# Kernel optimization log

Hardware: AMD Instinct MI355X
Metric: run time of the kernel (lower is better)

Reference implementation:

```python
import jax, jax.numpy as jnp
import numpy as np

M, K, N = 4096, 4096, 11008  # tokens, in_features, out_features
PACK = 8  # int4 nibbles per int32


def setup_inputs() -> dict:
    key = jax.random.key(0)
    k1, k2, k3, k4, k5 = jax.random.split(key, 5)
    x = jax.random.normal(k1, (M, K), dtype=jnp.float32)
    weights = jax.random.randint(k2, (N, K // PACK), 0, 2147483647, dtype=jnp.int32)
    # positive per-channel scales, small float zero offsets (GPTQ-style affine)
    scales = jax.random.uniform(k3, (N,), dtype=jnp.float32, minval=0.005, maxval=0.02)
    zeros = jax.random.normal(k4, (N,), dtype=jnp.float32) * 0.05
    bias = jax.random.normal(k5, (N,), dtype=jnp.float32) * 0.02
    return {"x": x, "weights": weights, "scales": scales, "zeros": zeros, "bias": bias}


def _unpack_int4(weights):
    # weights: [N, K//8] int32 -> nibbles [N, K] in [0, 15]
    shifts = jnp.arange(PACK, dtype=jnp.int32) * 4  # [8]
    nib = (weights[:, :, None] >> shifts[None, None, :]) & 0xF  # [N, K//8, 8]
    return nib.reshape(weights.shape[0], -1)  # [N, K]


def reference(x, weights, scales, zeros, bias):
    x_dtype = x.dtype
    xb = x.astype(jnp.bfloat16)
    q = _unpack_int4(weights).astype(jnp.bfloat16)  # [N, K]
    # dequant: w = q * scale + zero  (per output channel)
    w = q * scales.astype(jnp.bfloat16)[:, None] + zeros.astype(jnp.bfloat16)[:, None]
    out = jnp.einsum('mk,nk->mn', xb, w, preferred_element_type=jnp.float32)
    out = out + bias[None, :]
    return out.astype(x_dtype)
```

## Files before the change

### kernel.cpp

```cpp
#include <hip/hip_runtime.h>
#include <stdint.h>

#define MDIM 4096
#define KDIM 4096
#define NDIM 11008
#define KP   (KDIM/8)
#define NKT2 (KDIM/128)

typedef float  f32x4   __attribute__((ext_vector_type(4)));
typedef __bf16 bf16x8  __attribute__((ext_vector_type(8)));
typedef unsigned short u16x8 __attribute__((ext_vector_type(8)));
typedef int    i32x4   __attribute__((ext_vector_type(4)));
typedef int    i32x16  __attribute__((ext_vector_type(16)));
typedef char   c8x8    __attribute__((ext_vector_type(8)));
typedef char   c8x16   __attribute__((ext_vector_type(16)));

__device__ __forceinline__ unsigned short f2bf(float f) {
  uint32_t u = __builtin_bit_cast(uint32_t, f);
  u += 0x7FFFu + ((u >> 16) & 1u);
  return (unsigned short)(u >> 16);
}
__device__ __forceinline__ float bf2f(unsigned short h) {
  return __builtin_bit_cast(float, (uint32_t)h << 16);
}
__device__ __forceinline__ float bf16r(float f) { return bf2f(f2bf(f)); }

__device__ __forceinline__ void lds16(const void* g, void* l) {
  __builtin_amdgcn_global_load_lds(
      (const __attribute__((address_space(1))) unsigned int*)g,
      (__attribute__((address_space(3))) unsigned int*)l, 16, 0, 0);
}

__global__ __launch_bounds__(256) void repack_q_kernel(
    const uint32_t* __restrict__ wq, c8x8* __restrict__ Q8) {
  int idx = blockIdx.x * 256 + threadIdx.x;
  uint32_t w = wq[idx];
  c8x8 v;
#pragma unroll
  for (int j = 0; j < 8; ++j) v[j] = (char)((w >> (4 * j)) & 0xF);
  Q8[idx] = v;
}

__global__ __launch_bounds__(256) void quant_x_kernel(
    const float* __restrict__ x, c8x16* __restrict__ X8,
    float* __restrict__ delta, float* __restrict__ xsum) {
  __shared__ float red[256];
  const int row = blockIdx.x, t = threadIdx.x;
  const float4* xr = (const float4*)(x + (size_t)row * KDIM);
  float xb[16];
#pragma unroll
  for (int i = 0; i < 4; ++i) {
    float4 f = xr[t * 4 + i];
    xb[i * 4 + 0] = bf16r(f.x); xb[i * 4 + 1] = bf16r(f.y);
    xb[i * 4 + 2] = bf16r(f.z); xb[i * 4 + 3] = bf16r(f.w);
  }
  float mx = 0.f, sm = 0.f;
#pragma unroll
  for (int j = 0; j < 16; ++j) { mx = fmaxf(mx, fabsf(xb[j])); sm += xb[j]; }
  red[t] = mx; __syncthreads();
  for (int o = 128; o > 0; o >>= 1) {
    if (t < o) red[t] = fmaxf(red[t], red[t + o]);
    __syncthreads();
  }
  const float rmx = red[0];
  __syncthreads();
  red[t] = sm; __syncthreads();
  for (int o = 128; o > 0; o >>= 1) {
    if (t < o) red[t] += red[t + o];
    __syncthreads();
  }
  const float rsm = red[0];
  const float inv = (rmx > 0.f) ? 127.0f / rmx : 0.f;
  if (t == 0) {
    delta[row] = (rmx > 0.f) ? rmx / 127.0f : 0.f;
    xsum[row]  = rsm;
  }
  c8x16 q;
#pragma unroll
  for (int j = 0; j < 16; ++j) q[j] = (char)__float2int_rn(xb[j] * inv);
  X8[(size_t)row * 256 + t] = q;
}

__global__ __launch_bounds__(512, 2) void gemm256_i8_kernel(
    const char* __restrict__ A8, const char* __restrict__ Q8,
    const float* __restrict__ delta, const float* __restrict__ xsum,
    const float* __restrict__ scales, const float* __restrict__ zeros,
    const float* __restrict__ bias, float* __restrict__ out) {
  __shared__ __align__(16) char smem[131072];

  const int tid  = threadIdx.x;
  const int lane = tid & 63;
  const int wave = tid >> 6;
  const int wm   = wave >> 2;
  const int wn   = wave & 3;

  const int b   = blockIdx.x;
  const int swz = (b & 7) * 86 + (b >> 3);
  const int mt  = swz / 43;
  const int nt  = swz - mt * 43;
  const int bm0 = mt * 256, bn0 = nt * 256;

  const int srow   = lane >> 2;
  const int schunk = lane & 3;
  const int perm0  = schunk ^ (((srow >> 3) & 1) << 1);
  const int perm1  = perm0 ^ 1;
  const char* aR  = A8 + (size_t)(bm0 + wave * 32 + srow) * KDIM + perm0 * 16;
  const char* aR2 = A8 + (size_t)(bm0 + wave * 32 + 16 + srow) * KDIM + perm1 * 16;
  const char* bR  = Q8 + (size_t)(bn0 + wave * 32 + srow) * KDIM + perm0 * 16;
  const char* bR2 = Q8 + (size_t)(bn0 + wave * 32 + 16 + srow) * KDIM + perm1 * 16;

  const int r31 = lane & 31;
  const int sub = r31 >> 4;
  const int r15 = r31 & 15;
  const int hk  = lane >> 5;
  const int rd0 = sub * 1024 + r15 * 64 + ((hk ^ sub) << 4) + ((r15 & 8) << 2);
  const int rd1 = rd0 ^ 32;

  const int aoffc = wm * 8192;
  const int boffc = 65536 + wn * 4096;

  i32x16 acc[4][2];
#pragma unroll
  for (int i = 0; i < 4; ++i)
#pragma unroll
    for (int j = 0; j < 2; ++j)
#pragma unroll
      for (int r = 0; r < 16; ++r) acc[i][j][r] = 0;

  i32x4 Af[4], Bf[2];

#define STAGE_A(tile, h, slot)                                              \
  do {                                                                      \
    const size_t ko_ = (size_t)((tile) * 128 + (h) * 64);                   \
    char* d_ = smem + ((slot) << 14) + wave * 2048;                         \
    lds16(aR + ko_, d_);                                                    \
    lds16(aR2 + ko_, d_ + 1024);                                            \
  } while (0)

#define STAGE_B(tile, h, slot)                                              \
  do {                                                                      \
    const size_t ko_ = (size_t)((tile) * 128 + (h) * 64);                   \
    char* d_ = smem + 65536 + ((slot) << 14) + wave * 2048;                 \
    lds16(bR + ko_, d_);                                                    \
    lds16(bR2 + ko_, d_ + 1024);                                            \
  } while (0)

#define READ6(slotbase, S)                                                  \
  do {                                                                      \
    const int ro_ = (S) ? rd1 : rd0;                                        \
    _Pragma("unroll") for (int mf = 0; mf < 4; ++mf)                        \
        Af[mf] = *(const i32x4*)(smem + aoffc + (slotbase) +                \
                                 mf * 2048 + ro_);                          \
    _Pragma("unroll") for (int nf = 0; nf < 2; ++nf)                        \
        Bf[nf] = *(const i32x4*)(smem + boffc + (slotbase) +                \
                                 nf * 2048 + ro_);                          \
  } while (0)

#define MFMA8()                                                             \
  __builtin_amdgcn_s_setprio(1);                                            \
  _Pragma("unroll") for (int mf = 0; mf < 4; ++mf)                          \
      _Pragma("unroll") for (int nf = 0; nf < 2; ++nf)                      \
          acc[mf][nf] = __builtin_amdgcn_mfma_i32_32x32x32_i8(              \
              Af[mf], Bf[nf], acc[mf][nf], 0, 0, 0);                        \
  __builtin_amdgcn_s_setprio(0);

#define BAR                                                                 \
  __builtin_amdgcn_s_barrier();                                             \
  __builtin_amdgcn_sched_barrier(0);

#define VMWAIT(N) asm volatile("s_waitcnt vmcnt(" #N ")" ::: "memory")

#define TILE(T, S0s, S1s, SN1s, NSTG, VM1STMT, VM3STMT)                     \
  do {                                                                      \
    READ6((S0s) << 14, 0);                                                  \
    if ((NSTG) >= 1) STAGE_A((T) + 1, 1, SN1s);                             \
    BAR; MFMA8(); BAR;                                                      \
    READ6((S0s) << 14, 1);                                                  \
    if ((NSTG) >= 2) STAGE_B((T) + 1, 1, SN1s);                             \
    VM1STMT;                                                                \
    BAR; MFMA8(); BAR;                                                      \
    READ6((S1s) << 14, 0);                                                  \
    if ((NSTG) >= 3) STAGE_A((T) + 2, 0, S0s);                              \
    BAR; MFMA8(); BAR;                                                      \
    READ6((S1s) << 14, 1);                                                  \
    if ((NSTG) >= 4) STAGE_B((T) + 2, 0, S0s);                              \
    VM3STMT;                                                                \
    BAR; MFMA8(); BAR;                                                      \
  } while (0)

  STAGE_A(0, 0, 0);
  STAGE_B(0, 0, 0);
  STAGE_A(0, 1, 1);
  STAGE_B(0, 1, 1);
  STAGE_A(1, 0, 2);
  STAGE_B(1, 0, 2);
  VMWAIT(8);
  BAR;

  for (int tt = 0; tt < 30; tt += 2) {
    TILE(tt,     0, 1, 3, 4, VMWAIT(8), VMWAIT(8));
    TILE(tt + 1, 2, 3, 1, 4, VMWAIT(8), VMWAIT(8));
  }
  TILE(30, 0, 1, 3, 2, VMWAIT(8), VMWAIT(4));
  TILE(31, 2, 3, 1, 0, VMWAIT(0), (void)0);

#undef TILE
#undef VMWAIT
#undef BAR
#undef MFMA8
#undef READ6
#undef STAGE_B
#undef STAGE_A

  const int colv = bn0 + wn * 64 + (lane & 31);
  const int rowb = bm0 + wm * 128 + ((lane >> 5) << 2);
  float sb[2], zb[2], bv[2];
#pragma unroll
  for (int nf = 0; nf < 2; ++nf) {
    sb[nf] = bf16r(scales[colv + nf * 32]);
    zb[nf] = bf16r(zeros[colv + nf * 32]);
    bv[nf] = bias[colv + nf * 32];
  }
#pragma unroll
  for (int mf = 0; mf < 4; ++mf)
#pragma unroll
    for (int reg = 0; reg < 16; ++reg) {
      const int row = rowb + mf * 32 + (reg & 3) + ((reg >> 2) << 3);
      const float dm = delta[row];
      const float xm = xsum[row];
#pragma unroll
      for (int nf = 0; nf < 2; ++nf)
        out[(size_t)row * NDIM + colv + nf * 32] =
            (float)acc[mf][nf][reg] * (dm * sb[nf]) + (zb[nf] * xm + bv[nf]);
    }
}

__global__ __launch_bounds__(256, 3) void gemm_fused_kernel(
    const float* __restrict__ x, const uint32_t* __restrict__ wq,
    const float* __restrict__ scales, const float* __restrict__ zeros,
    const float* __restrict__ bias, float* __restrict__ out) {
  __shared__ __align__(16) char smem[2 * 128 * 64 * 2];
  char* As = smem;
  char* Bs = smem + 16384;

  const int tid  = threadIdx.x;
  const int lane = tid & 63;
  const int wave = tid >> 6;
  const int wm = wave >> 1, wn = wave & 1;

  const int b   = blockIdx.x;
  const int swz = (b & 7) * 344 + (b >> 3);
  const int mt  = swz / 86;
  const int nt  = swz - mt * 86;
  const int bm0 = mt * 128, bn0 = nt * 128;

  f32x4 acc[4][4];
#pragma unroll
  for (int i = 0; i < 4; ++i)
#pragma unroll
    for (int j = 0; j < 4; ++j) acc[i][j] = (f32x4){0.f, 0.f, 0.f, 0.f};

  const int base_a = ((wm * 64 + (lane & 15)) << 7) + ((lane >> 4) << 4);
  const int base_b = ((wn * 64 + (lane & 15)) << 7) + ((lane >> 4) << 4);

  float sv[4], zv[4];
#pragma unroll
  for (int it = 0; it < 4; ++it) {
    int r = bn0 + it * 32 + (tid >> 3);
    sv[it] = bf16r(scales[r]);
    zv[it] = bf16r(zeros[r]);
  }

  for (int kt = 0; kt < KDIM / 64; ++kt) {
    const int k0 = kt * 64;
    __syncthreads();
#pragma unroll
    for (int it = 0; it < 4; ++it) {
      int ch = it * 256 + tid;
      int row = ch >> 3, c8 = ch & 7;
      const float* src = x + (size_t)(bm0 + row) * KDIM + k0 + c8 * 8;
      float4 f0 = *(const float4*)src;
      float4 f1 = *(const float4*)(src + 4);
      u16x8 v;
      v[0] = f2bf(f0.x); v[1] = f2bf(f0.y); v[2] = f2bf(f0.z); v[3] = f2bf(f0.w);
      v[4] = f2bf(f1.x); v[5] = f2bf(f1.y); v[6] = f2bf(f1.z); v[7] = f2bf(f1.w);
      *(u16x8*)(As + row * 128 + c8 * 16) = v;
    }
#pragma unroll
    for (int it = 0; it < 4; ++it) {
      int ch = it * 256 + tid;
      int row = ch >> 3, kp = ch & 7;
      uint32_t w = wq[(size_t)(bn0 + row) * KP + kt * 8 + kp];
      float s = sv[it], z = zv[it];
      u16x8 v;
#pragma unroll
      for (int j = 0; j < 8; ++j) {
        float qf = (float)((w >> (4 * j)) & 0xF);
        float t  = bf16r(qf * s);
        v[j] = f2bf(t + z);
      }
      *(u16x8*)(Bs + row * 128 + kp * 16) = v;
    }
    __syncthreads();
#pragma unroll
    for (int ks = 0; ks < 2; ++ks) {
      bf16x8 af[4], bf[4];
#pragma unroll
      for (int i = 0; i < 4; ++i)
        af[i] = *(const bf16x8*)(As + base_a + i * 2048 + ks * 64);
#pragma unroll
      for (int j = 0; j < 4; ++j)
        bf[j] = *(const bf16x8*)(Bs + base_b + j * 2048 + ks * 64);
#pragma unroll
      for (int i = 0; i < 4; ++i)
#pragma unroll
        for (int j = 0; j < 4; ++j)
          acc[i][j] = __builtin_amdgcn_mfma_f32_16x16x32_bf16(af[i], bf[j],
                                                              acc[i][j], 0, 0, 0);
    }
  }

  const int colbase = bn0 + wn * 64 + (lane & 15);
  const int rowbase = bm0 + wm * 64 + ((lane >> 4) << 2);
  float bv[4];
#pragma unroll
  for (int j = 0; j < 4; ++j) bv[j] = bias[colbase + j * 16];
#pragma unroll
  for (int i = 0; i < 4; ++i) {
#pragma unroll
    for (int j = 0; j < 4; ++j) {
      size_t base = (size_t)(rowbase + i * 16) * NDIM + colbase + j * 16;
#pragma unroll
      for (int r = 0; r < 4; ++r)
        out[base + (size_t)r * NDIM] = acc[i][j][r] + bv[j];
    }
  }
}

extern "C" void kernel_launch(void* const* d_in, const int* in_sizes, int n_in,
                              void* d_out, int out_size, void* d_ws, size_t ws_size,
                              hipStream_t stream) {
  const float*    x      = (const float*)d_in[0];
  const uint32_t* wq     = (const uint32_t*)d_in[1];
  const float*    scales = (const float*)d_in[2];
  const float*    zeros  = (const float*)d_in[3];
  const float*    bias   = (const float*)d_in[4];
  float*          out    = (float*)d_out;

  const size_t offQ = 0;
  const size_t szQ  = (size_t)NDIM * KDIM;
  const size_t offX = szQ;
  const size_t szX  = (size_t)MDIM * KDIM;
  const size_t offD = offX + szX;
  const size_t offS = offD + MDIM * sizeof(float);
  const size_t need = offS + MDIM * sizeof(float);

  if (ws_size >= need) {
    char*  Q8    = (char*)d_ws + offQ;
    char*  X8    = (char*)d_ws + offX;
    float* dlt   = (float*)((char*)d_ws + offD);
    float* xsm   = (float*)((char*)d_ws + offS);
    repack_q_kernel<<<(NDIM * KP) / 256, 256, 0, stream>>>(wq, (c8x8*)Q8);
    quant_x_kernel<<<MDIM, 256, 0, stream>>>(x, (c8x16*)X8, dlt, xsm);
    gemm256_i8_kernel<<<688, 512, 0, stream>>>(X8, Q8, dlt, xsm, scales, zeros,
                                               bias, out);
  } else {
    gemm_fused_kernel<<<2752, 256, 0, stream>>>(x, wq, scales, zeros, bias, out);
  }
}
```

Before: 232.4 us.

## Shrink int8 GEMM block tile to 128x256 with triple-buffered LDS pipeline

Changes the int8 MFMA GEMM block tile from 256x256 to 128x256. Each wave now holds a 2x2 set of 32x32 accumulators instead of 4x2, and LDS use drops from 128KB to 72KB. The pipeline becomes a 3-slot rotation that prefetches one full K-tile ahead, and launch bounds ask for more resident blocks with twice as many blocks launched. The aim is higher occupancy and better wave balance across CUs, at the cost of more global traffic for B per output and a lower MFMA-to-load ratio per block.

```diff
diff --git a/kernel.cpp b/kernel.cpp
--- a/kernel.cpp
+++ b/kernel.cpp
@@ -5,7 +5,6 @@
 #define KDIM 4096
 #define NDIM 11008
 #define KP   (KDIM/8)
-#define NKT2 (KDIM/128)
 
 typedef float  f32x4   __attribute__((ext_vector_type(4)));
 typedef __bf16 bf16x8  __attribute__((ext_vector_type(8)));
@@ -81,12 +80,12 @@
   X8[(size_t)row * 256 + t] = q;
 }
 
-__global__ __launch_bounds__(512, 2) void gemm256_i8_kernel(
+__global__ __launch_bounds__(512, 4) void gemm_i8_kernel(
     const char* __restrict__ A8, const char* __restrict__ Q8,
     const float* __restrict__ delta, const float* __restrict__ xsum,
     const float* __restrict__ scales, const float* __restrict__ zeros,
     const float* __restrict__ bias, float* __restrict__ out) {
-  __shared__ __align__(16) char smem[131072];
+  __shared__ __align__(16) char smem[73728];
 
   const int tid  = threadIdx.x;
   const int lane = tid & 63;
@@ -95,19 +94,20 @@
   const int wn   = wave & 3;
 
   const int b   = blockIdx.x;
-  const int swz = (b & 7) * 86 + (b >> 3);
+  const int swz = (b & 7) * 172 + (b >> 3);
   const int mt  = swz / 43;
   const int nt  = swz - mt * 43;
-  const int bm0 = mt * 256, bn0 = nt * 256;
+  const int bm0 = mt * 128, bn0 = nt * 256;
 
   const int srow   = lane >> 2;
   const int schunk = lane & 3;
-  const int perm0  = schunk ^ (((srow >> 3) & 1) << 1);
-  const int perm1  = perm0 ^ 1;
-  const char* aR  = A8 + (size_t)(bm0 + wave * 32 + srow) * KDIM + perm0 * 16;
-  const char* aR2 = A8 + (size_t)(bm0 + wave * 32 + 16 + srow) * KDIM + perm1 * 16;
-  const char* bR  = Q8 + (size_t)(bn0 + wave * 32 + srow) * KDIM + perm0 * 16;
-  const char* bR2 = Q8 + (size_t)(bn0 + wave * 32 + 16 + srow) * KDIM + perm1 * 16;
+  const int p0c    = schunk ^ (((srow >> 3) & 1) << 1);
+  const char* aRw = A8 + (size_t)(bm0 + wave * 16 + srow) * KDIM
+                       + (size_t)((p0c ^ (wave & 1)) * 16);
+  const char* bR  = Q8 + (size_t)(bn0 + wave * 32 + srow) * KDIM
+                       + (size_t)(p0c * 16);
+  const char* bR2 = Q8 + (size_t)(bn0 + wave * 32 + 16 + srow) * KDIM
+                       + (size_t)((p0c ^ 1) * 16);
 
   const int r31 = lane & 31;
   const int sub = r31 >> 4;
@@ -116,49 +116,48 @@
   const int rd0 = sub * 1024 + r15 * 64 + ((hk ^ sub) << 4) + ((r15 & 8) << 2);
   const int rd1 = rd0 ^ 32;
 
-  const int aoffc = wm * 8192;
-  const int boffc = 65536 + wn * 4096;
-
-  i32x16 acc[4][2];
-#pragma unroll
-  for (int i = 0; i < 4; ++i)
+  const int apair = (wm << 1);
+  const int bpair = (wn << 1);
+
+  i32x16 acc[2][2];
+#pragma unroll
+  for (int i = 0; i < 2; ++i)
 #pragma unroll
     for (int j = 0; j < 2; ++j)
 #pragma unroll
       for (int r = 0; r < 16; ++r) acc[i][j][r] = 0;
 
-  i32x4 Af[4], Bf[2];
+  i32x4 Af[2], Bf[2];
+
+#define ABASE(S) ((S) * 8192)
+#define BBASE(S) (24576 + (S) * 16384)
 
 #define STAGE_A(tile, h, slot)                                              \
-  do {                                                                      \
-    const size_t ko_ = (size_t)((tile) * 128 + (h) * 64);                   \
-    char* d_ = smem + ((slot) << 14) + wave * 2048;                         \
-    lds16(aR + ko_, d_);                                                    \
-    lds16(aR2 + ko_, d_ + 1024);                                            \
-  } while (0)
+  lds16(aRw + (size_t)((tile) * 128 + (h) * 64),                            \
+        smem + ABASE(slot) + wave * 1024)
 
 #define STAGE_B(tile, h, slot)                                              \
   do {                                                                      \
     const size_t ko_ = (size_t)((tile) * 128 + (h) * 64);                   \
-    char* d_ = smem + 65536 + ((slot) << 14) + wave * 2048;                 \
+    char* d_ = smem + BBASE(slot) + wave * 2048;                            \
     lds16(bR + ko_, d_);                                                    \
     lds16(bR2 + ko_, d_ + 1024);                                            \
   } while (0)
 
-#define READ6(slotbase, S)                                                  \
+#define READ4(S, KS)                                                        \
   do {                                                                      \
-    const int ro_ = (S) ? rd1 : rd0;                                        \
-    _Pragma("unroll") for (int mf = 0; mf < 4; ++mf)                        \
-        Af[mf] = *(const i32x4*)(smem + aoffc + (slotbase) +                \
-                                 mf * 2048 + ro_);                          \
+    const int ro_ = (KS) ? rd1 : rd0;                                       \
+    _Pragma("unroll") for (int mf = 0; mf < 2; ++mf)                        \
+        Af[mf] = *(const i32x4*)(smem + ABASE(S) +                          \
+                                 (apair + mf) * 2048 + ro_);                \
     _Pragma("unroll") for (int nf = 0; nf < 2; ++nf)                        \
-        Bf[nf] = *(const i32x4*)(smem + boffc + (slotbase) +                \
-                                 nf * 2048 + ro_);                          \
+        Bf[nf] = *(const i32x4*)(smem + BBASE(S) +                          \
+                                 (bpair + nf) * 2048 + ro_);                \
   } while (0)
 
-#define MFMA8()                                                             \
+#define MFMA4()                                                             \
   __builtin_amdgcn_s_setprio(1);                                            \
-  _Pragma("unroll") for (int mf = 0; mf < 4; ++mf)                          \
+  _Pragma("unroll") for (int mf = 0; mf < 2; ++mf)                          \
       _Pragma("unroll") for (int nf = 0; nf < 2; ++nf)                      \
           acc[mf][nf] = __builtin_amdgcn_mfma_i32_32x32x32_i8(              \
               Af[mf], Bf[nf], acc[mf][nf], 0, 0, 0);                        \
@@ -170,50 +169,53 @@
 
 #define VMWAIT(N) asm volatile("s_waitcnt vmcnt(" #N ")" ::: "memory")
 
-#define TILE(T, S0s, S1s, SN1s, NSTG, VM1STMT, VM3STMT)                     \
+#define TILE(T, S0, S1, SA, STG01, STG23, VM1STMT, VM3STMT)                 \
   do {                                                                      \
-    READ6((S0s) << 14, 0);                                                  \
-    if ((NSTG) >= 1) STAGE_A((T) + 1, 1, SN1s);                             \
-    BAR; MFMA8(); BAR;                                                      \
-    READ6((S0s) << 14, 1);                                                  \
-    if ((NSTG) >= 2) STAGE_B((T) + 1, 1, SN1s);                             \
+    READ4(S0, 0);                                                           \
+    if (STG01) STAGE_A((T) + 1, 0, SA);                                     \
+    BAR; MFMA4(); BAR;                                                      \
+    READ4(S0, 1);                                                           \
+    if (STG01) STAGE_B((T) + 1, 0, SA);                                     \
     VM1STMT;                                                                \
-    BAR; MFMA8(); BAR;                                                      \
-    READ6((S1s) << 14, 0);                                                  \
-    if ((NSTG) >= 3) STAGE_A((T) + 2, 0, S0s);                              \
-    BAR; MFMA8(); BAR;                                                      \
-    READ6((S1s) << 14, 1);                                                  \
-    if ((NSTG) >= 4) STAGE_B((T) + 2, 0, S0s);                              \
+    BAR; MFMA4(); BAR;                                                      \
+    READ4(S1, 0);                                                           \
+    if (STG23) STAGE_A((T) + 1, 1, S0);                                     \
+    BAR; MFMA4(); BAR;                                                      \
+    READ4(S1, 1);                                                           \
+    if (STG23) STAGE_B((T) + 1, 1, S0);                                     \
     VM3STMT;                                                                \
-    BAR; MFMA8(); BAR;                                                      \
+    BAR; MFMA4(); BAR;                                                      \
   } while (0)
 
-  STAGE_A(0, 0, 0);
-  STAGE_B(0, 0, 0);
-  STAGE_A(0, 1, 1);
-  STAGE_B(0, 1, 1);
-  STAGE_A(1, 0, 2);
-  STAGE_B(1, 0, 2);
-  VMWAIT(8);
+  STAGE_A(0, 0, 0); STAGE_B(0, 0, 0);
+  STAGE_A(0, 1, 1); STAGE_B(0, 1, 1);
+  STAGE_A(1, 0, 2); STAGE_B(1, 0, 2);
+  VMWAIT(6);
   BAR;
 
-  for (int tt = 0; tt < 30; tt += 2) {
-    TILE(tt,     0, 1, 3, 4, VMWAIT(8), VMWAIT(8));
-    TILE(tt + 1, 2, 3, 1, 4, VMWAIT(8), VMWAIT(8));
-  }
-  TILE(30, 0, 1, 3, 2, VMWAIT(8), VMWAIT(4));
-  TILE(31, 2, 3, 1, 0, VMWAIT(0), (void)0);
+  TILE(0, 0, 1, 2, 0, 1, VMWAIT(3), VMWAIT(3));
+  for (int tt = 1; tt < 28; tt += 3) {
+    TILE(tt,     2, 0, 1, 1, 1, VMWAIT(3), VMWAIT(3));
+    TILE(tt + 1, 1, 2, 0, 1, 1, VMWAIT(3), VMWAIT(3));
+    TILE(tt + 2, 0, 1, 2, 1, 1, VMWAIT(3), VMWAIT(3));
+  }
+  TILE(28, 2, 0, 1, 1, 1, VMWAIT(3), VMWAIT(3));
+  TILE(29, 1, 2, 0, 1, 1, VMWAIT(3), VMWAIT(3));
+  TILE(30, 0, 1, 2, 1, 1, VMWAIT(3), VMWAIT(3));
+  TILE(31, 2, 0, 1, 0, 0, VMWAIT(0), (void)0);
 
 #undef TILE
 #undef VMWAIT
 #undef BAR
-#undef MFMA8
-#undef READ6
+#undef MFMA4
+#undef READ4
 #undef STAGE_B
 #undef STAGE_A
+#undef BBASE
+#undef ABASE
 
   const int colv = bn0 + wn * 64 + (lane & 31);
-  const int rowb = bm0 + wm * 128 + ((lane >> 5) << 2);
+  const int rowb = bm0 + wm * 64 + ((lane >> 5) << 2);
   float sb[2], zb[2], bv[2];
 #pragma unroll
   for (int nf = 0; nf < 2; ++nf) {
@@ -222,7 +224,7 @@
     bv[nf] = bias[colv + nf * 32];
   }
 #pragma unroll
-  for (int mf = 0; mf < 4; ++mf)
+  for (int mf = 0; mf < 2; ++mf)
 #pragma unroll
     for (int reg = 0; reg < 16; ++reg) {
       const int row = rowb + mf * 32 + (reg & 3) + ((reg >> 2) << 3);
@@ -362,8 +364,8 @@
     float* xsm   = (float*)((char*)d_ws + offS);
     repack_q_kernel<<<(NDIM * KP) / 256, 256, 0, stream>>>(wq, (c8x8*)Q8);
     quant_x_kernel<<<MDIM, 256, 0, stream>>>(x, (c8x16*)X8, dlt, xsm);
-    gemm256_i8_kernel<<<688, 512, 0, stream>>>(X8, Q8, dlt, xsm, scales, zeros,
-                                               bias, out);
+    gemm_i8_kernel<<<1376, 512, 0, stream>>>(X8, Q8, dlt, xsm, scales, zeros,
+                                             bias, out);
   } else {
     gemm_fused_kernel<<<2752, 256, 0, stream>>>(x, wq, scales, zeros, bias, out);
   }
```

Result: slower. 285.4 us (+22.8%).

## Use 4 waves with 128x128 per-wave tiles in int8 GEMM

Applied to the files above, without the earlier changes.

Restructures the 256x256 int8 MFMA GEMM from 8 waves (each 128x64) to 4 waves (each 128x128). Each wave now stages 64 rows of A and B per half-tile and issues 16 MFMAs per LDS read phase instead of 8. This raises register reuse of fragments and cuts LDS traffic per MFMA. The cost is a doubled accumulator footprint (256 VGPRs of accumulators), launch bounds of one block per SM-slot, and fewer waves to hide latency.

```diff
diff --git a/kernel.cpp b/kernel.cpp
--- a/kernel.cpp
+++ b/kernel.cpp
@@ -5,7 +5,6 @@
 #define KDIM 4096
 #define NDIM 11008
 #define KP   (KDIM/8)
-#define NKT2 (KDIM/128)
 
 typedef float  f32x4   __attribute__((ext_vector_type(4)));
 typedef __bf16 bf16x8  __attribute__((ext_vector_type(8)));
@@ -81,7 +80,7 @@
   X8[(size_t)row * 256 + t] = q;
 }
 
-__global__ __launch_bounds__(512, 2) void gemm256_i8_kernel(
+__global__ __launch_bounds__(256, 1) void gemm_i8_kernel(
     const char* __restrict__ A8, const char* __restrict__ Q8,
     const float* __restrict__ delta, const float* __restrict__ xsum,
     const float* __restrict__ scales, const float* __restrict__ zeros,
@@ -91,8 +90,8 @@
   const int tid  = threadIdx.x;
   const int lane = tid & 63;
   const int wave = tid >> 6;
-  const int wm   = wave >> 2;
-  const int wn   = wave & 3;
+  const int wm   = wave >> 1;
+  const int wn   = wave & 1;
 
   const int b   = blockIdx.x;
   const int swz = (b & 7) * 86 + (b >> 3);
@@ -102,12 +101,11 @@
 
   const int srow   = lane >> 2;
   const int schunk = lane & 3;
-  const int perm0  = schunk ^ (((srow >> 3) & 1) << 1);
-  const int perm1  = perm0 ^ 1;
-  const char* aR  = A8 + (size_t)(bm0 + wave * 32 + srow) * KDIM + perm0 * 16;
-  const char* aR2 = A8 + (size_t)(bm0 + wave * 32 + 16 + srow) * KDIM + perm1 * 16;
-  const char* bR  = Q8 + (size_t)(bn0 + wave * 32 + srow) * KDIM + perm0 * 16;
-  const char* bR2 = Q8 + (size_t)(bn0 + wave * 32 + 16 + srow) * KDIM + perm1 * 16;
+  const int p0c    = schunk ^ (((srow >> 3) & 1) << 1);
+  const char* aRe = A8 + (size_t)(bm0 + wave * 64 + srow) * KDIM + (size_t)(p0c * 16);
+  const char* aRo = A8 + (size_t)(bm0 + wave * 64 + srow) * KDIM + (size_t)((p0c ^ 1) * 16);
+  const char* bRe = Q8 + (size_t)(bn0 + wave * 64 + srow) * KDIM + (size_t)(p0c * 16);
+  const char* bRo = Q8 + (size_t)(bn0 + wave * 64 + srow) * KDIM + (size_t)((p0c ^ 1) * 16);
 
   const int r31 = lane & 31;
   const int sub = r31 >> 4;
@@ -117,49 +115,56 @@
   const int rd1 = rd0 ^ 32;
 
   const int aoffc = wm * 8192;
-  const int boffc = 65536 + wn * 4096;
-
-  i32x16 acc[4][2];
+  const int boffc = 65536 + wn * 8192;
+
+  i32x16 acc[4][4];
 #pragma unroll
   for (int i = 0; i < 4; ++i)
 #pragma unroll
-    for (int j = 0; j < 2; ++j)
+    for (int j = 0; j < 4; ++j)
 #pragma unroll
       for (int r = 0; r < 16; ++r) acc[i][j][r] = 0;
 
-  i32x4 Af[4], Bf[2];
+  i32x4 Af[4], Bf[4];
+
+#define ABASE(S) ((S) << 14)
+#define BBASE(S) (65536 + ((S) << 14))
 
 #define STAGE_A(tile, h, slot)                                              \
   do {                                                                      \
     const size_t ko_ = (size_t)((tile) * 128 + (h) * 64);                   \
-    char* d_ = smem + ((slot) << 14) + wave * 2048;                         \
-    lds16(aR + ko_, d_);                                                    \
-    lds16(aR2 + ko_, d_ + 1024);                                            \
+    char* d_ = smem + ABASE(slot) + wave * 4096;                            \
+    lds16(aRe + ko_,                        d_);                            \
+    lds16(aRo + (size_t)16 * KDIM + ko_,    d_ + 1024);                     \
+    lds16(aRe + (size_t)32 * KDIM + ko_,    d_ + 2048);                     \
+    lds16(aRo + (size_t)48 * KDIM + ko_,    d_ + 3072);                     \
   } while (0)
 
 #define STAGE_B(tile, h, slot)                                              \
   do {                                                                      \
     const size_t ko_ = (size_t)((tile) * 128 + (h) * 64);                   \
-    char* d_ = smem + 65536 + ((slot) << 14) + wave * 2048;                 \
-    lds16(bR + ko_, d_);                                                    \
-    lds16(bR2 + ko_, d_ + 1024);                                            \
+    char* d_ = smem + BBASE(slot) + wave * 4096;                            \
+    lds16(bRe + ko_,                        d_);                            \
+    lds16(bRo + (size_t)16 * KDIM + ko_,    d_ + 1024);                     \
+    lds16(bRe + (size_t)32 * KDIM + ko_,    d_ + 2048);                     \
+    lds16(bRo + (size_t)48 * KDIM + ko_,    d_ + 3072);                     \
   } while (0)
 
-#define READ6(slotbase, S)                                                  \
+#define READ8(S, KS)                                                        \
   do {                                                                      \
-    const int ro_ = (S) ? rd1 : rd0;                                        \
+    const int ro_ = (KS) ? rd1 : rd0;                                       \
     _Pragma("unroll") for (int mf = 0; mf < 4; ++mf)                        \
-        Af[mf] = *(const i32x4*)(smem + aoffc + (slotbase) +                \
+        Af[mf] = *(const i32x4*)(smem + aoffc + ABASE(S) +                  \
                                  mf * 2048 + ro_);                          \
-    _Pragma("unroll") for (int nf = 0; nf < 2; ++nf)                        \
-        Bf[nf] = *(const i32x4*)(smem + boffc + (slotbase) +                \
+    _Pragma("unroll") for (int nf = 0; nf < 4; ++nf)                        \
+        Bf[nf] = *(const i32x4*)(smem + boffc + ((S) << 14) +               \
                                  nf * 2048 + ro_);                          \
   } while (0)
 
-#define MFMA8()                                                             \
+#define MFMA16()                                                            \
   __builtin_amdgcn_s_setprio(1);                                            \
   _Pragma("unroll") for (int mf = 0; mf < 4; ++mf)                          \
-      _Pragma("unroll") for (int nf = 0; nf < 2; ++nf)                      \
+      _Pragma("unroll") for (int nf = 0; nf < 4; ++nf)                      \
           acc[mf][nf] = __builtin_amdgcn_mfma_i32_32x32x32_i8(              \
               Af[mf], Bf[nf], acc[mf][nf], 0, 0, 0);                        \
   __builtin_amdgcn_s_setprio(0);
@@ -172,51 +177,50 @@
 
 #define TILE(T, S0s, S1s, SN1s, NSTG, VM1STMT, VM3STMT)                     \
   do {                                                                      \
-    READ6((S0s) << 14, 0);                                                  \
+    READ8(S0s, 0);                                                          \
     if ((NSTG) >= 1) STAGE_A((T) + 1, 1, SN1s);                             \
-    BAR; MFMA8(); BAR;                                                      \
-    READ6((S0s) << 14, 1);                                                  \
+    BAR; MFMA16(); BAR;                                                     \
+    READ8(S0s, 1);                                                          \
     if ((NSTG) >= 2) STAGE_B((T) + 1, 1, SN1s);                             \
     VM1STMT;                                                                \
-    BAR; MFMA8(); BAR;                                                      \
-    READ6((S1s) << 14, 0);                                                  \
+    BAR; MFMA16(); BAR;                                                     \
+    READ8(S1s, 0);                                                          \
     if ((NSTG) >= 3) STAGE_A((T) + 2, 0, S0s);                              \
-    BAR; MFMA8(); BAR;                                                      \
-    READ6((S1s) << 14, 1);                                                  \
+    BAR; MFMA16(); BAR;                                                     \
+    READ8(S1s, 1);                                                          \
     if ((NSTG) >= 4) STAGE_B((T) + 2, 0, S0s);                              \
     VM3STMT;                                                                \
-    BAR; MFMA8(); BAR;                                                      \
+    BAR; MFMA16(); BAR;                                                     \
   } while (0)
 
-  STAGE_A(0, 0, 0);
-  STAGE_B(0, 0, 0);
-  STAGE_A(0, 1, 1);
-  STAGE_B(0, 1, 1);
-  STAGE_A(1, 0, 2);
-  STAGE_B(1, 0, 2);
-  VMWAIT(8);
+  STAGE_A(0, 0, 0); STAGE_B(0, 0, 0);
+  STAGE_A(0, 1, 1); STAGE_B(0, 1, 1);
+  STAGE_A(1, 0, 2); STAGE_B(1, 0, 2);
+  VMWAIT(16);
   BAR;
 
   for (int tt = 0; tt < 30; tt += 2) {
-    TILE(tt,     0, 1, 3, 4, VMWAIT(8), VMWAIT(8));
-    TILE(tt + 1, 2, 3, 1, 4, VMWAIT(8), VMWAIT(8));
-  }
-  TILE(30, 0, 1, 3, 2, VMWAIT(8), VMWAIT(4));
+    TILE(tt,     0, 1, 3, 4, VMWAIT(16), VMWAIT(16));
+    TILE(tt + 1, 2, 3, 1, 4, VMWAIT(16), VMWAIT(16));
+  }
+  TILE(30, 0, 1, 3, 2, VMWAIT(16), VMWAIT(8));
   TILE(31, 2, 3, 1, 0, VMWAIT(0), (void)0);
 
 #undef TILE
 #undef VMWAIT
 #undef BAR
-#undef MFMA8
-#undef READ6
+#undef MFMA16
+#undef READ8
 #undef STAGE_B
 #undef STAGE_A
-
-  const int colv = bn0 + wn * 64 + (lane & 31);
+#undef BBASE
+#undef ABASE
+
+  const int colv = bn0 + wn * 128 + (lane & 31);
   const int rowb = bm0 + wm * 128 + ((lane >> 5) << 2);
-  float sb[2], zb[2], bv[2];
-#pragma unroll
-  for (int nf = 0; nf < 2; ++nf) {
+  float sb[4], zb[4], bv[4];
+#pragma unroll
+  for (int nf = 0; nf < 4; ++nf) {
     sb[nf] = bf16r(scales[colv + nf * 32]);
     zb[nf] = bf16r(zeros[colv + nf * 32]);
     bv[nf] = bias[colv + nf * 32];
@@ -229,7 +233,7 @@
       const float dm = delta[row];
       const float xm = xsum[row];
 #pragma unroll
-      for (int nf = 0; nf < 2; ++nf)
+      for (int nf = 0; nf < 4; ++nf)
         out[(size_t)row * NDIM + colv + nf * 32] =
             (float)acc[mf][nf][reg] * (dm * sb[nf]) + (zb[nf] * xm + bv[nf]);
     }
@@ -362,8 +366,8 @@
     float* xsm   = (float*)((char*)d_ws + offS);
     repack_q_kernel<<<(NDIM * KP) / 256, 256, 0, stream>>>(wq, (c8x8*)Q8);
     quant_x_kernel<<<MDIM, 256, 0, stream>>>(x, (c8x16*)X8, dlt, xsm);
-    gemm256_i8_kernel<<<688, 512, 0, stream>>>(X8, Q8, dlt, xsm, scales, zeros,
-                                               bias, out);
+    gemm_i8_kernel<<<688, 256, 0, stream>>>(X8, Q8, dlt, xsm, scales, zeros,
+                                            bias, out);
   } else {
     gemm_fused_kernel<<<2752, 256, 0, stream>>>(x, wq, scales, zeros, bias, out);
   }
```

New measurement: 234.2 us. Within noise of the previous version (+0.8%).

## Shrink int8 GEMM block tile to 256x128 with 4 waves and 3-slot pipeline

Applied to the files above, without the earlier changes.

Switches the int8 MFMA GEMM from 512-thread 256x256 tiles to 256-thread 256x128 tiles with 1376 blocks. Each wave now stages four A row-groups, and the shared-memory ring becomes three 24KB slots, each holding one half-K-tile of A and B, rotated over a 3-tile unrolled loop. The smaller LDS footprint (72KB) is meant to let more blocks co-reside and to balance the grid better across CUs. The cost is lower arithmetic intensity per block, meaning more global and L2 traffic for A reloads.

```diff
diff --git a/kernel.cpp b/kernel.cpp
--- a/kernel.cpp
+++ b/kernel.cpp
@@ -5,7 +5,6 @@
 #define KDIM 4096
 #define NDIM 11008
 #define KP   (KDIM/8)
-#define NKT2 (KDIM/128)
 
 typedef float  f32x4   __attribute__((ext_vector_type(4)));
 typedef __bf16 bf16x8  __attribute__((ext_vector_type(8)));
@@ -81,33 +80,32 @@
   X8[(size_t)row * 256 + t] = q;
 }
 
-__global__ __launch_bounds__(512, 2) void gemm256_i8_kernel(
+__global__ __launch_bounds__(256, 2) void gemm_i8_kernel(
     const char* __restrict__ A8, const char* __restrict__ Q8,
     const float* __restrict__ delta, const float* __restrict__ xsum,
     const float* __restrict__ scales, const float* __restrict__ zeros,
     const float* __restrict__ bias, float* __restrict__ out) {
-  __shared__ __align__(16) char smem[131072];
+  __shared__ __align__(16) char smem[73728];
 
   const int tid  = threadIdx.x;
   const int lane = tid & 63;
   const int wave = tid >> 6;
-  const int wm   = wave >> 2;
-  const int wn   = wave & 3;
+  const int wm   = wave >> 1;
+  const int wn   = wave & 1;
 
   const int b   = blockIdx.x;
-  const int swz = (b & 7) * 86 + (b >> 3);
-  const int mt  = swz / 43;
-  const int nt  = swz - mt * 43;
-  const int bm0 = mt * 256, bn0 = nt * 256;
+  const int swz = (b & 7) * 172 + (b >> 3);
+  const int mt  = swz / 86;
+  const int nt  = swz - mt * 86;
+  const int bm0 = mt * 256, bn0 = nt * 128;
 
   const int srow   = lane >> 2;
   const int schunk = lane & 3;
-  const int perm0  = schunk ^ (((srow >> 3) & 1) << 1);
-  const int perm1  = perm0 ^ 1;
-  const char* aR  = A8 + (size_t)(bm0 + wave * 32 + srow) * KDIM + perm0 * 16;
-  const char* aR2 = A8 + (size_t)(bm0 + wave * 32 + 16 + srow) * KDIM + perm1 * 16;
-  const char* bR  = Q8 + (size_t)(bn0 + wave * 32 + srow) * KDIM + perm0 * 16;
-  const char* bR2 = Q8 + (size_t)(bn0 + wave * 32 + 16 + srow) * KDIM + perm1 * 16;
+  const int p0c    = schunk ^ (((srow >> 3) & 1) << 1);
+  const char* aRe = A8 + (size_t)(bm0 + wave * 64 + srow) * KDIM + (size_t)(p0c * 16);
+  const char* aRo = A8 + (size_t)(bm0 + wave * 64 + srow) * KDIM + (size_t)((p0c ^ 1) * 16);
+  const char* bRe = Q8 + (size_t)(bn0 + wave * 32 + srow) * KDIM + (size_t)(p0c * 16);
+  const char* bRo = Q8 + (size_t)(bn0 + wave * 32 + 16 + srow) * KDIM + (size_t)((p0c ^ 1) * 16);
 
   const int r31 = lane & 31;
   const int sub = r31 >> 4;
@@ -116,9 +114,6 @@
   const int rd0 = sub * 1024 + r15 * 64 + ((hk ^ sub) << 4) + ((r15 & 8) << 2);
   const int rd1 = rd0 ^ 32;
 
-  const int aoffc = wm * 8192;
-  const int boffc = 65536 + wn * 4096;
-
   i32x16 acc[4][2];
 #pragma unroll
   for (int i = 0; i < 4; ++i)
@@ -129,30 +124,33 @@
 
   i32x4 Af[4], Bf[2];
 
-#define STAGE_A(tile, h, slot)                                              \
+#define SLOTB(S) ((S) * 24576)
+
+#define STAGE_A(t, h, S)                                                    \
   do {                                                                      \
-    const size_t ko_ = (size_t)((tile) * 128 + (h) * 64);                   \
-    char* d_ = smem + ((slot) << 14) + wave * 2048;                         \
-    lds16(aR + ko_, d_);                                                    \
-    lds16(aR2 + ko_, d_ + 1024);                                            \
+    const size_t ko_ = (size_t)(t) * 128 + (size_t)(h) * 64;                \
+    char* d_ = smem + SLOTB(S) + wave * 4096;                               \
+    _Pragma("unroll") for (int j = 0; j < 4; ++j)                           \
+      lds16(((j & 1) ? aRo : aRe) + (size_t)j * 16 * KDIM + ko_,            \
+            d_ + j * 1024);                                                 \
   } while (0)
 
-#define STAGE_B(tile, h, slot)                                              \
+#define STAGE_B(t, h, S)                                                    \
   do {                                                                      \
-    const size_t ko_ = (size_t)((tile) * 128 + (h) * 64);                   \
-    char* d_ = smem + 65536 + ((slot) << 14) + wave * 2048;                 \
-    lds16(bR + ko_, d_);                                                    \
-    lds16(bR2 + ko_, d_ + 1024);                                            \
+    const size_t ko_ = (size_t)(t) * 128 + (size_t)(h) * 64;                \
+    char* d_ = smem + SLOTB(S) + 16384 + wave * 2048;                       \
+    lds16(bRe + ko_, d_);                                                   \
+    lds16(bRo + ko_, d_ + 1024);                                            \
   } while (0)
 
-#define READ6(slotbase, S)                                                  \
+#define READ6(S, KS)                                                        \
   do {                                                                      \
-    const int ro_ = (S) ? rd1 : rd0;                                        \
+    const int ro_ = (KS) ? rd1 : rd0;                                       \
     _Pragma("unroll") for (int mf = 0; mf < 4; ++mf)                        \
-        Af[mf] = *(const i32x4*)(smem + aoffc + (slotbase) +                \
+        Af[mf] = *(const i32x4*)(smem + SLOTB(S) + wm * 8192 +              \
                                  mf * 2048 + ro_);                          \
     _Pragma("unroll") for (int nf = 0; nf < 2; ++nf)                        \
-        Bf[nf] = *(const i32x4*)(smem + boffc + (slotbase) +                \
+        Bf[nf] = *(const i32x4*)(smem + SLOTB(S) + 16384 + wn * 4096 +      \
                                  nf * 2048 + ro_);                          \
   } while (0)
 
@@ -170,39 +168,40 @@
 
 #define VMWAIT(N) asm volatile("s_waitcnt vmcnt(" #N ")" ::: "memory")
 
-#define TILE(T, S0s, S1s, SN1s, NSTG, VM1STMT, VM3STMT)                     \
+#define TILE(T, S0, S1, SA, STG01, STG23, VM1STMT, VM3STMT)                 \
   do {                                                                      \
-    READ6((S0s) << 14, 0);                                                  \
-    if ((NSTG) >= 1) STAGE_A((T) + 1, 1, SN1s);                             \
+    READ6(S0, 0);                                                           \
+    if (STG01) STAGE_A((T) + 1, 0, SA);                                     \
     BAR; MFMA8(); BAR;                                                      \
-    READ6((S0s) << 14, 1);                                                  \
-    if ((NSTG) >= 2) STAGE_B((T) + 1, 1, SN1s);                             \
+    READ6(S0, 1);                                                           \
+    if (STG01) STAGE_B((T) + 1, 0, SA);                                     \
     VM1STMT;                                                                \
     BAR; MFMA8(); BAR;                                                      \
-    READ6((S1s) << 14, 0);                                                  \
-    if ((NSTG) >= 3) STAGE_A((T) + 2, 0, S0s);                              \
+    READ6(S1, 0);                                                           \
+    if (STG23) STAGE_A((T) + 1, 1, S0);                                     \
     BAR; MFMA8(); BAR;                                                      \
-    READ6((S1s) << 14, 1);                                                  \
-    if ((NSTG) >= 4) STAGE_B((T) + 2, 0, S0s);                              \
+    READ6(S1, 1);                                                           \
+    if (STG23) STAGE_B((T) + 1, 1, S0);                                     \
     VM3STMT;                                                                \
     BAR; MFMA8(); BAR;                                                      \
   } while (0)
 
-  STAGE_A(0, 0, 0);
-  STAGE_B(0, 0, 0);
-  STAGE_A(0, 1, 1);
-  STAGE_B(0, 1, 1);
-  STAGE_A(1, 0, 2);
-  STAGE_B(1, 0, 2);
-  VMWAIT(8);
+  STAGE_A(0, 0, 0); STAGE_B(0, 0, 0);
+  STAGE_A(0, 1, 1); STAGE_B(0, 1, 1);
+  STAGE_A(1, 0, 2); STAGE_B(1, 0, 2);
+  VMWAIT(12);
   BAR;
 
-  for (int tt = 0; tt < 30; tt += 2) {
-    TILE(tt,     0, 1, 3, 4, VMWAIT(8), VMWAIT(8));
-    TILE(tt + 1, 2, 3, 1, 4, VMWAIT(8), VMWAIT(8));
-  }
-  TILE(30, 0, 1, 3, 2, VMWAIT(8), VMWAIT(4));
-  TILE(31, 2, 3, 1, 0, VMWAIT(0), (void)0);
+  TILE(0, 0, 1, 2, 0, 1, VMWAIT(6), VMWAIT(6));
+  for (int tt = 1; tt < 28; tt += 3) {
+    TILE(tt,     2, 0, 1, 1, 1, VMWAIT(6), VMWAIT(6));
+    TILE(tt + 1, 1, 2, 0, 1, 1, VMWAIT(6), VMWAIT(6));
+    TILE(tt + 2, 0, 1, 2, 1, 1, VMWAIT(6), VMWAIT(6));
+  }
+  TILE(28, 2, 0, 1, 1, 1, VMWAIT(6), VMWAIT(6));
+  TILE(29, 1, 2, 0, 1, 1, VMWAIT(6), VMWAIT(6));
+  TILE(30, 0, 1, 2, 1, 1, VMWAIT(6), VMWAIT(6));
+  TILE(31, 2, 0, 1, 0, 0, VMWAIT(0), (void)0);
 
 #undef TILE
 #undef VMWAIT
@@ -211,6 +210,7 @@
 #undef READ6
 #undef STAGE_B
 #undef STAGE_A
+#undef SLOTB
 
   const int colv = bn0 + wn * 64 + (lane & 31);
   const int rowb = bm0 + wm * 128 + ((lane >> 5) << 2);
@@ -362,8 +362,8 @@
     float* xsm   = (float*)((char*)d_ws + offS);
     repack_q_kernel<<<(NDIM * KP) / 256, 256, 0, stream>>>(wq, (c8x8*)Q8);
     quant_x_kernel<<<MDIM, 256, 0, stream>>>(x, (c8x16*)X8, dlt, xsm);
-    gemm256_i8_kernel<<<688, 512, 0, stream>>>(X8, Q8, dlt, xsm, scales, zeros,
-                                               bias, out);
+    gemm_i8_kernel<<<1376, 256, 0, stream>>>(X8, Q8, dlt, xsm, scales, zeros,
+                                             bias, out);
   } else {
     gemm_fused_kernel<<<2752, 256, 0, stream>>>(x, wq, scales, zeros, bias, out);
   }
```

New measurement: 239.8 us. 3.2% more time.
